# Kernel optimization log

Measured on AMD Instinct MI355X. Metric: run time of the kernel, lower is better.

The kernel has to match this reference:

```python
import jax, jax.numpy as jnp
import numpy as np

NUM_STEPS = 151
STEP = 2.0 / (NUM_STEPS - 1)
TSIZE = NUM_STEPS  # t = -1, -1+step, ..., 1
N = 4096
D = 512
NUM_CLASSES = 100


def setup_inputs() -> dict:
    key = jax.random.key(0)
    k1, k2 = jax.random.split(key)
    feats = jax.random.normal(k1, (N, D), dtype=jnp.float32)
    # L2-normalize so pairwise dot products lie in [-1, 1] (histogram support)
    feats = feats / jnp.linalg.norm(feats, axis=1, keepdims=True)
    classes = jax.random.randint(k2, (N,), 0, NUM_CLASSES, dtype=jnp.int64)
    return {"features": feats, "classes": classes}


def reference(features, classes):
    n = features.shape[0]
    # pairwise cosine similarities, upper triangle (i < j)
    dists = features @ features.T  # [N, N]
    iu, ju = jnp.triu_indices(n, k=1)  # static index arrays
    s = dists[iu, ju]                  # [P] similarities
    pos = classes[iu] == classes[ju]   # [P] same-class mask

    # triangular soft-binning exactly as in the torch code:
    # f = floor(s/step)*step; bin at t==f gets (s-f)/step, bin at t==f+step gets (f+step-s)/step
    f = jnp.floor(s / STEP) * STEP
    j = jnp.floor(s / STEP).astype(jnp.int32) + (NUM_STEPS - 1) // 2  # index of t == f
    wa = (s - f) / STEP
    wb = (f + STEP - s) / STEP
    va = (j >= 0) & (j < TSIZE)
    vb = (j + 1 >= 0) & (j + 1 < TSIZE)
    ja = jnp.clip(j, 0, TSIZE - 1)
    jb = jnp.clip(j + 1, 0, TSIZE - 1)

    def hist(mask, size):
        w_a = jnp.where(va & mask, wa, 0.0)
        w_b = jnp.where(vb & mask, wb, 0.0)
        h = jnp.zeros(TSIZE, s.dtype).at[ja].add(w_a).at[jb].add(w_b)
        return h / size.astype(s.dtype)

    pos_size = pos.sum()
    neg_size = (~pos).sum()
    hist_pos = hist(pos, pos_size)
    hist_neg = hist(~pos, neg_size)
    # tril-masked repeat + sum(0) == inclusive cumulative sum of hist_pos
    hist_pos_cdf = jnp.cumsum(hist_pos)
    loss = jnp.sum(hist_neg * hist_pos_cdf)
    return loss
```

## Files before the change

kernel.cpp:

```cpp
#include <hip/hip_runtime.h>


#define N_PTS   4096
#define DIM     512
#define TSIZE   151
#define HALF_T  75
#define BM      128
#define BK      32
#define NTILES  32
#define NBLOCKS 528
#define P_TOTAL 8386560u
#define STEPF   (2.0f / 150.0f)
#define STEPINV 75.0f
#define NCOPY   16
#define NCOPY_FB 8
#define HSTRIDE 309

typedef short bfrag __attribute__((ext_vector_type(8)));
typedef float ffrag __attribute__((ext_vector_type(4)));
typedef unsigned short u16;
typedef unsigned int   u32;

__device__ __forceinline__ ffrag mfma16(bfrag a, bfrag b, ffrag c) {
  return __builtin_amdgcn_mfma_f32_16x16x32_bf16(a, b, c, 0, 0, 0);
}

__device__ __forceinline__ void split4(float4 v, uint2* hi, uint2* lo) {
  u32 u0 = __float_as_uint(v.x), u1 = __float_as_uint(v.y);
  u32 u2 = __float_as_uint(v.z), u3 = __float_as_uint(v.w);
  float r0 = v.x - __uint_as_float(u0 & 0xFFFF0000u);
  float r1 = v.y - __uint_as_float(u1 & 0xFFFF0000u);
  float r2 = v.z - __uint_as_float(u2 & 0xFFFF0000u);
  float r3 = v.w - __uint_as_float(u3 & 0xFFFF0000u);
  hi->x = (u0 >> 16) | (u1 & 0xFFFF0000u);
  hi->y = (u2 >> 16) | (u3 & 0xFFFF0000u);
  lo->x = (__float_as_uint(r0) >> 16) | (__float_as_uint(r1) & 0xFFFF0000u);
  lo->y = (__float_as_uint(r2) >> 16) | (__float_as_uint(r3) & 0xFFFF0000u);
}

__device__ __forceinline__ void bin_epilogue(
    const ffrag (&acc)[4][4], float* h, const int* clsA, const int* clsB,
    int wy, int wx, int l4, int l16, bool diag, u32* myPos)
{
  #pragma unroll
  for (int fi = 0; fi < 4; ++fi) {
    #pragma unroll
    for (int fj = 0; fj < 4; ++fj) {
      #pragma unroll
      for (int r = 0; r < 4; ++r) {
        int li = wy * 64 + fi * 16 + l4 * 4 + r;
        int lj = wx * 64 + fj * 16 + l16;
        if (diag && li >= lj) continue;
        float s  = acc[fi][fj][r];
        float jf = floorf(s * STEPINV);
        int   jb = (int)jf + HALF_T;
        float f  = jf * STEPF;
        float wa = (s - f) * STEPINV;
        float wb = (f + STEPF - s) * STEPINV;
        bool  pos = (clsA[li] == clsB[lj]);
        *myPos += pos ? 1u : 0u;
        int off = pos ? 0 : TSIZE;
        if (jb >= 0 && jb < TSIZE)         unsafeAtomicAdd(h + off + jb, wa);
        if (jb + 1 >= 0 && jb + 1 < TSIZE) unsafeAtomicAdd(h + off + jb + 1, wb);
      }
    }
  }
}

__device__ __forceinline__ void tile_decode(int orig, int* bi_, int* bj_) {
  int sbid = (orig & 7) * 66 + (orig >> 3);
  int rem = sbid, cnt = NTILES, bi = 0;
  while (rem >= cnt) { rem -= cnt; --cnt; ++bi; }
  *bi_ = bi; *bj_ = bi + rem;
}

__global__ __launch_bounds__(256) void presplit(
    const float* __restrict__ F, u16* __restrict__ FhiP, u16* __restrict__ FloP)
{
  int u = blockIdx.x * 256 + threadIdx.x;
  int kb = u >> 12, row = u & 4095;
  const float* src = F + (size_t)row * DIM + kb * 8;
  float4 v0 = *(const float4*)(src);
  float4 v1 = *(const float4*)(src + 4);
  uint2 h0, l0, h1, l1;
  split4(v0, &h0, &l0);
  split4(v1, &h1, &l1);
  uint4 hv; hv.x = h0.x; hv.y = h0.y; hv.z = h1.x; hv.w = h1.y;
  uint4 lv; lv.x = l0.x; lv.y = l0.y; lv.z = l1.x; lv.w = l1.y;
  *(uint4*)(FhiP + (size_t)u * 8) = hv;
  *(uint4*)(FloP + (size_t)u * 8) = lv;
}

__global__ __launch_bounds__(256, 3) void hist_mfma(
    const u16* __restrict__ FhiP, const u16* __restrict__ FloP,
    const int* __restrict__ cls,
    float* __restrict__ g_hist, u32* __restrict__ g_pos)
{
  __shared__ float hist[NCOPY * HSTRIDE];
  __shared__ int clsA[BM], clsB[BM];
  __shared__ u32 posCount;

  const int t = threadIdx.x;
  int bi, bj;
  tile_decode((int)blockIdx.x, &bi, &bj);
  const int rowA = bi * BM, rowB = bj * BM;

  for (int i = t; i < NCOPY * HSTRIDE; i += 256) hist[i] = 0.0f;
  if (t < BM) clsA[t] = cls[rowA + t];
  else        clsB[t - BM] = cls[rowB + (t - BM)];
  if (t == 0) posCount = 0u;

  const int lane = t & 63, w = t >> 6;
  const int wy = w >> 1, wx = w & 1;
  const int l4 = lane >> 4, l16 = lane & 15;

  ffrag acc[4][4] = {};

  const size_t arow = (size_t)(rowA + wy * 64 + l16);
  const size_t brow = (size_t)(rowB + wx * 64 + l16);

  for (int s = 0; s < DIM / 32; ++s) {
    const size_t kbase = (size_t)(s * 4 + l4) * N_PTS;
    const u16* aph = FhiP + (kbase + arow) * 8;
    const u16* apl = FloP + (kbase + arow) * 8;
    const u16* bph = FhiP + (kbase + brow) * 8;
    const u16* bpl = FloP + (kbase + brow) * 8;
    bfrag ah[4], al[4];
    #pragma unroll
    for (int fi = 0; fi < 4; ++fi) {
      ah[fi] = *(const bfrag*)(aph + fi * 128);
      al[fi] = *(const bfrag*)(apl + fi * 128);
    }
    #pragma unroll
    for (int fj = 0; fj < 4; ++fj) {
      bfrag bh = *(const bfrag*)(bph + fj * 128);
      bfrag bl = *(const bfrag*)(bpl + fj * 128);
      #pragma unroll
      for (int fi = 0; fi < 4; ++fi) {
        acc[fi][fj] = mfma16(ah[fi], bh, acc[fi][fj]);
        acc[fi][fj] = mfma16(al[fi], bh, acc[fi][fj]);
        acc[fi][fj] = mfma16(ah[fi], bl, acc[fi][fj]);
      }
    }
  }

  __syncthreads();
  u32 myPos = 0;
  float* h = hist + l16 * HSTRIDE;
  bin_epilogue(acc, h, clsA, clsB, wy, wx, l4, l16, bi == bj, &myPos);
  atomicAdd(&posCount, myPos);
  __syncthreads();

  for (int i = t; i < 2 * TSIZE; i += 256) {
    float v = 0.0f;
    #pragma unroll
    for (int c = 0; c < NCOPY; ++c) v += hist[c * HSTRIDE + i];
    unsafeAtomicAdd(g_hist + i, v);
  }
  if (t == 0) atomicAdd(g_pos, posCount);
}

__global__ __launch_bounds__(256, 3) void hist_fb(
    const float* __restrict__ F, const int* __restrict__ cls,
    float* __restrict__ g_hist, u32* __restrict__ g_pos)
{
  __shared__ __align__(16) u16 Ahi[BM * BK];
  __shared__ __align__(16) u16 Alo[BM * BK];
  __shared__ __align__(16) u16 Bhi[BM * BK];
  __shared__ __align__(16) u16 Blo[BM * BK];
  __shared__ float hist[NCOPY_FB * HSTRIDE];
  __shared__ int clsA[BM], clsB[BM];
  __shared__ u32 posCount;

  const int t = threadIdx.x;
  int bi, bj;
  tile_decode((int)blockIdx.x, &bi, &bj);
  const int rowA = bi * BM, rowB = bj * BM;

  for (int i = t; i < NCOPY_FB * HSTRIDE; i += 256) hist[i] = 0.0f;
  if (t < BM) clsA[t] = cls[rowA + t];
  else        clsB[t - BM] = cls[rowB + (t - BM)];
  if (t == 0) posCount = 0u;

  const int lane = t & 63, w = t >> 6;
  const int wy = w >> 1, wx = w & 1;
  const int l4 = lane >> 4, l16 = lane & 15;

  ffrag acc[4][4] = {};

  for (int kk = 0; kk < DIM; kk += BK) {
    __syncthreads();
    #pragma unroll
    for (int m = 0; m < 4; ++m) {
      int q  = t + m * 256;
      int r  = q >> 3;
      int kq = (q & 7) * 4;
      float4 va = *(const float4*)(F + (size_t)(rowA + r) * DIM + kk + kq);
      float4 vb = *(const float4*)(F + (size_t)(rowB + r) * DIM + kk + kq);
      uint2 h, l;
      split4(va, &h, &l);
      *(uint2*)&Ahi[r * BK + kq] = h;
      *(uint2*)&Alo[r * BK + kq] = l;
      split4(vb, &h, &l);
      *(uint2*)&Bhi[r * BK + kq] = h;
      *(uint2*)&Blo[r * BK + kq] = l;
    }
    __syncthreads();

    bfrag ah[4], al[4];
    #pragma unroll
    for (int fi = 0; fi < 4; ++fi) {
      int off = (wy * 64 + fi * 16 + l16) * BK + l4 * 8;
      ah[fi] = *(const bfrag*)&Ahi[off];
      al[fi] = *(const bfrag*)&Alo[off];
    }
    #pragma unroll
    for (int fj = 0; fj < 4; ++fj) {
      int off = (wx * 64 + fj * 16 + l16) * BK + l4 * 8;
      bfrag bh = *(const bfrag*)&Bhi[off];
      bfrag bl = *(const bfrag*)&Blo[off];
      #pragma unroll
      for (int fi = 0; fi < 4; ++fi) {
        acc[fi][fj] = mfma16(ah[fi], bh, acc[fi][fj]);
        acc[fi][fj] = mfma16(al[fi], bh, acc[fi][fj]);
        acc[fi][fj] = mfma16(ah[fi], bl, acc[fi][fj]);
      }
    }
  }

  __syncthreads();
  u32 myPos = 0;
  float* h = hist + (lane & 7) * HSTRIDE;
  bin_epilogue(acc, h, clsA, clsB, wy, wx, l4, l16, bi == bj, &myPos);
  atomicAdd(&posCount, myPos);
  __syncthreads();

  for (int i = t; i < 2 * TSIZE; i += 256) {
    float v = 0.0f;
    #pragma unroll
    for (int c = 0; c < NCOPY_FB; ++c) v += hist[c * HSTRIDE + i];
    unsafeAtomicAdd(g_hist + i, v);
  }
  if (t == 0) atomicAdd(g_pos, posCount);
}

__global__ void zero_ws(float* g_hist, u32* g_pos) {
  int t = threadIdx.x;
  if (t < 2 * TSIZE) g_hist[t] = 0.0f;
  if (t == 0) *g_pos = 0u;
}

__global__ __launch_bounds__(256) void finalize(
    const float* __restrict__ g_hist,
    const u32* __restrict__ g_pos,
    float* __restrict__ out)
{
  __shared__ float hp[TSIZE];
  __shared__ float hn[TSIZE];
  __shared__ float red[4];
  const int t = threadIdx.x;
  const float Np = (float)(*g_pos);
  const float Nn = (float)(P_TOTAL - *g_pos);
  if (t < TSIZE) {
    hp[t] = g_hist[t] / Np;
    hn[t] = g_hist[TSIZE + t] / Nn;
  }
  __syncthreads();
  for (int off = 1; off < TSIZE; off <<= 1) {
    float v = 0.0f;
    if (t < TSIZE && t >= off) v = hp[t - off];
    __syncthreads();
    if (t < TSIZE) hp[t] += v;
    __syncthreads();
  }
  float term = (t < TSIZE) ? hn[t] * hp[t] : 0.0f;
  #pragma unroll
  for (int o = 32; o > 0; o >>= 1) term += __shfl_down(term, o);
  if ((t & 63) == 0) red[t >> 6] = term;
  __syncthreads();
  if (t == 0) *out = red[0] + red[1] + red[2] + red[3];
}

extern "C" void kernel_launch(void* const* d_in, const int* in_sizes, int n_in,
                              void* d_out, int out_size, void* d_ws, size_t ws_size,
                              hipStream_t stream) {
  const float* F   = (const float*)d_in[0];
  const int*   cls = (const int*)d_in[1];
  float* g_hist = (float*)d_ws;
  u32*   g_pos  = (u32*)((char*)d_ws + 2 * TSIZE * sizeof(float));
  float* out = (float*)d_out;

  const size_t offH   = 65536;
  const size_t bytesP = (size_t)N_PTS * DIM * sizeof(u16);

  zero_ws<<<1, 512, 0, stream>>>(g_hist, g_pos);
  if (ws_size >= offH + 2 * bytesP) {
    u16* FhiP = (u16*)((char*)d_ws + offH);
    u16* FloP = (u16*)((char*)d_ws + offH + bytesP);
    presplit<<<(N_PTS * DIM / 8) / 256, 256, 0, stream>>>(F, FhiP, FloP);
    hist_mfma<<<NBLOCKS, 256, 0, stream>>>(FhiP, FloP, cls, g_hist, g_pos);
  } else {
    hist_fb<<<NBLOCKS, 256, 0, stream>>>(F, cls, g_hist, g_pos);
  }
  finalize<<<1, 256, 0, stream>>>(g_hist, g_pos, out);
}
```

Baseline: 220.3 us.

## Double-buffer register fragment loads in MFMA histogram kernel and fuse workspace zeroing

Measured after the change: 215.3 us. 1.02x faster.

```diff
diff --git a/kernel.cpp b/kernel.cpp
--- a/kernel.cpp
+++ b/kernel.cpp
@@ -6,14 +6,12 @@
 #define TSIZE   151
 #define HALF_T  75
 #define BM      128
-#define BK      32
 #define NTILES  32
 #define NBLOCKS 528
 #define P_TOTAL 8386560u
 #define STEPF   (2.0f / 150.0f)
 #define STEPINV 75.0f
 #define NCOPY   16
-#define NCOPY_FB 8
 #define HSTRIDE 309
 
 typedef short bfrag __attribute__((ext_vector_type(8)));
@@ -75,10 +73,11 @@
 }
 
 __global__ __launch_bounds__(256) void presplit(
-    const float* __restrict__ F, u16* __restrict__ FhiP, u16* __restrict__ FloP)
+    const float* __restrict__ F, u16* __restrict__ FhiP, u16* __restrict__ FloP,
+    float* __restrict__ g_hist, u32* __restrict__ g_pos)
 {
   int u = blockIdx.x * 256 + threadIdx.x;
-  int kb = u >> 12, row = u & 4095;
+  int row = u >> 6, kb = u & 63;
   const float* src = F + (size_t)row * DIM + kb * 8;
   float4 v0 = *(const float4*)(src);
   float4 v1 = *(const float4*)(src + 4);
@@ -87,11 +86,16 @@
   split4(v1, &h1, &l1);
   uint4 hv; hv.x = h0.x; hv.y = h0.y; hv.z = h1.x; hv.w = h1.y;
   uint4 lv; lv.x = l0.x; lv.y = l0.y; lv.z = l1.x; lv.w = l1.y;
-  *(uint4*)(FhiP + (size_t)u * 8) = hv;
-  *(uint4*)(FloP + (size_t)u * 8) = lv;
-}
-
-__global__ __launch_bounds__(256, 3) void hist_mfma(
+  size_t dst = ((size_t)kb * N_PTS + row) * 8;
+  *(uint4*)(FhiP + dst) = hv;
+  *(uint4*)(FloP + dst) = lv;
+  if (blockIdx.x == 0) {
+    for (int i = threadIdx.x; i < 2 * TSIZE; i += 256) g_hist[i] = 0.0f;
+    if (threadIdx.x == 0) *g_pos = 0u;
+  }
+}
+
+__global__ __launch_bounds__(256, 2) void hist_mfma(
     const u16* __restrict__ FhiP, const u16* __restrict__ FloP,
     const int* __restrict__ cls,
     float* __restrict__ g_hist, u32* __restrict__ g_pos)
@@ -116,33 +120,53 @@
 
   ffrag acc[4][4] = {};
 
-  const size_t arow = (size_t)(rowA + wy * 64 + l16);
-  const size_t brow = (size_t)(rowB + wx * 64 + l16);
-
-  for (int s = 0; s < DIM / 32; ++s) {
-    const size_t kbase = (size_t)(s * 4 + l4) * N_PTS;
-    const u16* aph = FhiP + (kbase + arow) * 8;
-    const u16* apl = FloP + (kbase + arow) * 8;
-    const u16* bph = FhiP + (kbase + brow) * 8;
-    const u16* bpl = FloP + (kbase + brow) * 8;
-    bfrag ah[4], al[4];
-    #pragma unroll
-    for (int fi = 0; fi < 4; ++fi) {
-      ah[fi] = *(const bfrag*)(aph + fi * 128);
-      al[fi] = *(const bfrag*)(apl + fi * 128);
-    }
-    #pragma unroll
-    for (int fj = 0; fj < 4; ++fj) {
-      bfrag bh = *(const bfrag*)(bph + fj * 128);
-      bfrag bl = *(const bfrag*)(bpl + fj * 128);
-      #pragma unroll
-      for (int fi = 0; fi < 4; ++fi) {
-        acc[fi][fj] = mfma16(ah[fi], bh, acc[fi][fj]);
-        acc[fi][fj] = mfma16(al[fi], bh, acc[fi][fj]);
-        acc[fi][fj] = mfma16(ah[fi], bl, acc[fi][fj]);
-      }
-    }
-  }
+  const size_t SSTR = (size_t)4 * N_PTS * 8;
+  const size_t lb   = (size_t)l4 * N_PTS * 8;
+  const size_t ao   = lb + (size_t)(rowA + wy * 64 + l16) * 8;
+  const size_t bo   = lb + (size_t)(rowB + wx * 64 + l16) * 8;
+  const u16* pAh = FhiP + ao;
+  const u16* pAl = FloP + ao;
+  const u16* pBh = FhiP + bo;
+  const u16* pBl = FloP + bo;
+
+#define LOADF(ah, al, bh, bl, P)                                   \
+  do {                                                             \
+    _Pragma("unroll") for (int f = 0; f < 4; ++f) {                \
+      ah[f] = *(const bfrag*)(pAh + (P) * SSTR + f * 128);         \
+      al[f] = *(const bfrag*)(pAl + (P) * SSTR + f * 128);         \
+      bh[f] = *(const bfrag*)(pBh + (P) * SSTR + f * 128);         \
+      bl[f] = *(const bfrag*)(pBl + (P) * SSTR + f * 128);         \
+    }                                                              \
+  } while (0)
+
+#define COMPUTE(ah, al, bh, bl)                                    \
+  do {                                                             \
+    _Pragma("unroll") for (int fj = 0; fj < 4; ++fj)               \
+      _Pragma("unroll") for (int fi = 0; fi < 4; ++fi) {           \
+        acc[fi][fj] = mfma16(ah[fi], bh[fj], acc[fi][fj]);         \
+        acc[fi][fj] = mfma16(al[fi], bh[fj], acc[fi][fj]);         \
+        acc[fi][fj] = mfma16(ah[fi], bl[fj], acc[fi][fj]);         \
+      }                                                            \
+  } while (0)
+
+  bfrag a0h[4], a0l[4], b0h[4], b0l[4];
+  bfrag a1h[4], a1l[4], b1h[4], b1l[4];
+
+  LOADF(a0h, a0l, b0h, b0l, 0);
+  #pragma unroll 1
+  for (int s = 0; s < 7; ++s) {
+    LOADF(a1h, a1l, b1h, b1l, 1);
+    COMPUTE(a0h, a0l, b0h, b0l);
+    LOADF(a0h, a0l, b0h, b0l, 2);
+    COMPUTE(a1h, a1l, b1h, b1l);
+    pAh += 2 * SSTR; pAl += 2 * SSTR; pBh += 2 * SSTR; pBl += 2 * SSTR;
+  }
+  LOADF(a1h, a1l, b1h, b1l, 1);
+  COMPUTE(a0h, a0l, b0h, b0l);
+  COMPUTE(a1h, a1l, b1h, b1l);
+
+#undef LOADF
+#undef COMPUTE
 
   __syncthreads();
   u32 myPos = 0;
@@ -158,96 +182,6 @@
     unsafeAtomicAdd(g_hist + i, v);
   }
   if (t == 0) atomicAdd(g_pos, posCount);
-}
-
-__global__ __launch_bounds__(256, 3) void hist_fb(
-    const float* __restrict__ F, const int* __restrict__ cls,
-    float* __restrict__ g_hist, u32* __restrict__ g_pos)
-{
-  __shared__ __align__(16) u16 Ahi[BM * BK];
-  __shared__ __align__(16) u16 Alo[BM * BK];
-  __shared__ __align__(16) u16 Bhi[BM * BK];
-  __shared__ __align__(16) u16 Blo[BM * BK];
-  __shared__ float hist[NCOPY_FB * HSTRIDE];
-  __shared__ int clsA[BM], clsB[BM];
-  __shared__ u32 posCount;
-
-  const int t = threadIdx.x;
-  int bi, bj;
-  tile_decode((int)blockIdx.x, &bi, &bj);
-  const int rowA = bi * BM, rowB = bj * BM;
-
-  for (int i = t; i < NCOPY_FB * HSTRIDE; i += 256) hist[i] = 0.0f;
-  if (t < BM) clsA[t] = cls[rowA + t];
-  else        clsB[t - BM] = cls[rowB + (t - BM)];
-  if (t == 0) posCount = 0u;
-
-  const int lane = t & 63, w = t >> 6;
-  const int wy = w >> 1, wx = w & 1;
-  const int l4 = lane >> 4, l16 = lane & 15;
-
-  ffrag acc[4][4] = {};
-
-  for (int kk = 0; kk < DIM; kk += BK) {
-    __syncthreads();
-    #pragma unroll
-    for (int m = 0; m < 4; ++m) {
-      int q  = t + m * 256;
-      int r  = q >> 3;
-      int kq = (q & 7) * 4;
-      float4 va = *(const float4*)(F + (size_t)(rowA + r) * DIM + kk + kq);
-      float4 vb = *(const float4*)(F + (size_t)(rowB + r) * DIM + kk + kq);
-      uint2 h, l;
-      split4(va, &h, &l);
-      *(uint2*)&Ahi[r * BK + kq] = h;
-      *(uint2*)&Alo[r * BK + kq] = l;
-      split4(vb, &h, &l);
-      *(uint2*)&Bhi[r * BK + kq] = h;
-      *(uint2*)&Blo[r * BK + kq] = l;
-    }
-    __syncthreads();
-
-    bfrag ah[4], al[4];
-    #pragma unroll
-    for (int fi = 0; fi < 4; ++fi) {
-      int off = (wy * 64 + fi * 16 + l16) * BK + l4 * 8;
-      ah[fi] = *(const bfrag*)&Ahi[off];
-      al[fi] = *(const bfrag*)&Alo[off];
-    }
-    #pragma unroll
-    for (int fj = 0; fj < 4; ++fj) {
-      int off = (wx * 64 + fj * 16 + l16) * BK + l4 * 8;
-      bfrag bh = *(const bfrag*)&Bhi[off];
-      bfrag bl = *(const bfrag*)&Blo[off];
-      #pragma unroll
-      for (int fi = 0; fi < 4; ++fi) {
-        acc[fi][fj] = mfma16(ah[fi], bh, acc[fi][fj]);
-        acc[fi][fj] = mfma16(al[fi], bh, acc[fi][fj]);
-        acc[fi][fj] = mfma16(ah[fi], bl, acc[fi][fj]);
-      }
-    }
-  }
-
-  __syncthreads();
-  u32 myPos = 0;
-  float* h = hist + (lane & 7) * HSTRIDE;
-  bin_epilogue(acc, h, clsA, clsB, wy, wx, l4, l16, bi == bj, &myPos);
-  atomicAdd(&posCount, myPos);
-  __syncthreads();
-
-  for (int i = t; i < 2 * TSIZE; i += 256) {
-    float v = 0.0f;
-    #pragma unroll
-    for (int c = 0; c < NCOPY_FB; ++c) v += hist[c * HSTRIDE + i];
-    unsafeAtomicAdd(g_hist + i, v);
-  }
-  if (t == 0) atomicAdd(g_pos, posCount);
-}
-
-__global__ void zero_ws(float* g_hist, u32* g_pos) {
-  int t = threadIdx.x;
-  if (t < 2 * TSIZE) g_hist[t] = 0.0f;
-  if (t == 0) *g_pos = 0u;
 }
 
 __global__ __launch_bounds__(256) void finalize(
@@ -291,16 +225,10 @@
   float* out = (float*)d_out;
 
   const size_t offH   = 65536;
-  const size_t bytesP = (size_t)N_PTS * DIM * sizeof(u16);
-
-  zero_ws<<<1, 512, 0, stream>>>(g_hist, g_pos);
-  if (ws_size >= offH + 2 * bytesP) {
-    u16* FhiP = (u16*)((char*)d_ws + offH);
-    u16* FloP = (u16*)((char*)d_ws + offH + bytesP);
-    presplit<<<(N_PTS * DIM / 8) / 256, 256, 0, stream>>>(F, FhiP, FloP);
-    hist_mfma<<<NBLOCKS, 256, 0, stream>>>(FhiP, FloP, cls, g_hist, g_pos);
-  } else {
-    hist_fb<<<NBLOCKS, 256, 0, stream>>>(F, cls, g_hist, g_pos);
-  }
+  u16* FhiP = (u16*)((char*)d_ws + offH);
+  u16* FloP = (u16*)((char*)d_ws + offH + (size_t)N_PTS * DIM * sizeof(u16));
+
+  presplit<<<(N_PTS * 64) / 256, 256, 0, stream>>>(F, FhiP, FloP, g_hist, g_pos);
+  hist_mfma<<<NBLOCKS, 256, 0, stream>>>(FhiP, FloP, cls, g_hist, g_pos);
   finalize<<<1, 256, 0, stream>>>(g_hist, g_pos, out);
 }
```
